# Kernel tuning notes

Measured on AMD Instinct MI355X. Metric: run time of the kernel, lower is better.

## Reference

```python
import jax, jax.numpy as jnp
import numpy as np

DIM = 192
HEADS = 6
WIN = 64  # 8*8
EPS = 1e-12


def setup_inputs() -> dict:
    key = jax.random.key(0)
    ks = jax.random.split(key, 10)
    s = 0.02
    return {
        "qx": jax.random.normal(ks[0], (8192, WIN, DIM), jnp.float32),
        "kvx": jax.random.normal(ks[1], (4096, WIN, DIM), jnp.float32),
        "pos": jax.random.normal(ks[2], (1, WIN, DIM), jnp.float32) * s,
        "Wq": jax.random.normal(ks[3], (DIM, DIM), jnp.float32) * s,
        "bq": jnp.zeros((DIM,), jnp.float32),
        "Wkv": jax.random.normal(ks[4], (2 * DIM, DIM), jnp.float32) * s,
        "bkv": jnp.zeros((2 * DIM,), jnp.float32),
        "Wp": jax.random.normal(ks[5], (DIM, DIM), jnp.float32) * s,
        "bp": jnp.zeros((DIM,), jnp.float32),
    }


def _l2norm(x):
    # F.normalize: x / max(||x||_2, eps) along last dim
    n = jnp.sqrt(jnp.sum(x * x, axis=-1, keepdims=True))
    return x / jnp.maximum(n, EPS)


def reference(qx, kvx, pos, Wq, bq, Wkv, bkv, Wp, bp):
    B_q, q_len, C = qx.shape
    B_kv, kv_len, _ = kvx.shape
    tile_num = B_q // B_kv
    kvx = jnp.tile(kvx, (tile_num, 1, 1))
    qx = qx + pos
    q = qx @ Wq.T + bq                       # [Bq, q, C]
    kv = kvx @ Wkv.T + bkv                   # [Bq, kv, 2C]
    k, v = kv[..., :C], kv[..., C:]
    hd = C // HEADS
    q = q.reshape(B_q, q_len, HEADS, hd).transpose(0, 2, 1, 3)
    k = k.reshape(B_q, kv_len, HEADS, hd).transpose(0, 2, 1, 3)
    v = v.reshape(B_q, kv_len, HEADS, hd).transpose(0, 2, 1, 3)
    scale = 1.0 / np.sqrt(C).astype(np.float32)
    attn = jnp.einsum("bhqd,bhkd->bhqk", _l2norm(q), _l2norm(k)) * scale
    attn = jax.nn.softmax(attn, axis=-1)
    x = jnp.einsum("bhqk,bhkd->bhqd", attn, v)
    x = x.transpose(0, 2, 1, 3).reshape(B_q, q_len, C)
    return x @ Wp.T + bp
```

## Files before the change

### kernel.cpp

```cpp
#include <hip/hip_runtime.h>
#include <hip/hip_bf16.h>

#define TPB   512
#define CDIM  192
#define LDA   200
#define LDST  200
#define SCALE 0.07216878364870323f
#define EPSF  1e-12f

using short8 = __attribute__((ext_vector_type(8))) short;
using f32x4  = __attribute__((ext_vector_type(4))) float;
using us4    = __attribute__((ext_vector_type(4))) unsigned short;

__device__ __forceinline__ unsigned short hc(float f) {
  __hip_bfloat16 h = __float2bfloat16(f);
  unsigned short u; __builtin_memcpy(&u, &h, 2); return u;
}
__device__ __forceinline__ unsigned pack2(float x, float y) {
  return (unsigned)hc(x) | ((unsigned)hc(y) << 16);
}
#define MFMA(a, b, c) __builtin_amdgcn_mfma_f32_16x16x32_bf16((a), (b), (c), 0, 0, 0)
#define SCHED_FENCE() __builtin_amdgcn_sched_barrier(0)

#define NWQ  36864
#define NWKV 73728
#define NWP  36864
__global__ void cvt_weights(const float* __restrict__ Wq, const float* __restrict__ Wkv,
                            const float* __restrict__ Wp, unsigned short* __restrict__ o) {
  int i = blockIdx.x * blockDim.x + threadIdx.x;
  if (i < NWQ) o[i] = hc(Wq[i]);
  else if (i < NWQ + NWKV) o[i] = hc(Wkv[i - NWQ]);
  else if (i < NWQ + NWKV + NWP) o[i] = hc(Wp[i - NWQ - NWKV]);
}

__global__ __launch_bounds__(TPB, 4) void wa_v14(
    const float* __restrict__ qx, const float* __restrict__ kvx,
    const float* __restrict__ pos,
    const float* __restrict__ bq, const float* __restrict__ bkv,
    const float* __restrict__ bp,
    const unsigned short* __restrict__ Wqb, const unsigned short* __restrict__ Wkvb,
    const unsigned short* __restrict__ Wpb,
    float* __restrict__ out, int BKV, int tile_num)
{
  __shared__ __align__(16) unsigned short sA[64 * LDA];
  __shared__ __align__(16) unsigned short sU[64 * LDST];

  const int tid = threadIdx.x;
  const int wid = tid >> 6;
  const int l15 = (tid & 63) & 15;
  const int l4  = (tid & 63) >> 4;
  const int b   = blockIdx.x;
  const size_t kvoff = (size_t)b * (64 * CDIM);

  const int srcA = l15 + 32 * (l4 & 1);
  const int srcB = srcA + 16;
  const int sel  = l4 >> 1;
  auto redistC = [&](f32x4 cA, f32x4 cB) -> short8 {
    unsigned iA0 = pack2(cA[0], cA[1]), iA1 = pack2(cA[2], cA[3]);
    unsigned iB0 = pack2(cB[0], cB[1]), iB1 = pack2(cB[2], cB[3]);
    unsigned A00 = (unsigned)__shfl((int)iA0, srcA);
    unsigned A01 = (unsigned)__shfl((int)iA1, srcA);
    unsigned A10 = (unsigned)__shfl((int)iB0, srcA);
    unsigned A11 = (unsigned)__shfl((int)iB1, srcA);
    unsigned B00 = (unsigned)__shfl((int)iA0, srcB);
    unsigned B01 = (unsigned)__shfl((int)iA1, srcB);
    unsigned B10 = (unsigned)__shfl((int)iB0, srcB);
    unsigned B11 = (unsigned)__shfl((int)iB1, srcB);
    union { uint4 u; short8 s; } uu;
    uu.u.x = sel ? A10 : A00;
    uu.u.y = sel ? A11 : A01;
    uu.u.z = sel ? B10 : B00;
    uu.u.w = sel ? B11 : B01;
    return uu.s;
  };

  auto stage_q = [&](size_t qo) {
    const float4* gq = (const float4*)(qx + qo);
    const float4* p4 = (const float4*)pos;
    #pragma unroll
    for (int t = 0; t < 6; ++t) {
      int e = tid + t * TPB, row = e / 48, c4 = e % 48;
      float4 a = gq[e], p = p4[e];
      us4 wq;
      wq.x = hc(a.x + p.x); wq.y = hc(a.y + p.y); wq.z = hc(a.z + p.z); wq.w = hc(a.w + p.w);
      *(us4*)&sA[row * LDA + c4 * 4] = wq;
    }
  };

  stage_q(kvoff );
  {
    const float4* gk = (const float4*)(kvx + kvoff);
    #pragma unroll
    for (int t = 0; t < 6; ++t) {
      int e = tid + t * TPB, row = e / 48, c4 = e % 48;
      float4 k = gk[e];
      us4 wk; wk.x = hc(k.x); wk.y = hc(k.y); wk.z = hc(k.z); wk.w = hc(k.w);
      *(us4*)&sU[row * LDST + c4 * 4] = wk;
    }
  }
  __syncthreads();

  const int h = wid;

  short8 kres[4];
  short8 av[2][2];
  if (wid < 6) {
    {
      f32x4 kacc[4][2];
      #pragma unroll
      for (int mh = 0; mh < 2; ++mh) {
        float4 bk = *(const float4*)&bkv[32 * h + 16 * mh + 4 * l4];
        #pragma unroll
        for (int n = 0; n < 4; ++n) kacc[n][mh] = f32x4{bk.x, bk.y, bk.z, bk.w};
      }
      #pragma unroll
      for (int ks = 0; ks < 6; ++ks) {
        short8 act[4];
        #pragma unroll
        for (int n = 0; n < 4; ++n)
          act[n] = *(const short8*)&sU[(16 * n + l15) * LDST + ks * 32 + 8 * l4];
        #pragma unroll
        for (int mh = 0; mh < 2; ++mh) {
          short8 kw = *(const short8*)&Wkvb[(size_t)(32 * h + 16 * mh + l15) * CDIM + ks * 32 + 8 * l4];
          #pragma unroll
          for (int n = 0; n < 4; ++n) kacc[n][mh] = MFMA(kw, act[n], kacc[n][mh]);
        }
      }
      #pragma unroll
      for (int n = 0; n < 4; ++n) {
        float ss = 0.f;
        #pragma unroll
        for (int mh = 0; mh < 2; ++mh)
          #pragma unroll
          for (int r = 0; r < 4; ++r) ss += kacc[n][mh][r] * kacc[n][mh][r];
        ss += __shfl_xor(ss, 16);
        ss += __shfl_xor(ss, 32);
        float sc = 1.0f / fmaxf(sqrtf(ss), EPSF);
        #pragma unroll
        for (int mh = 0; mh < 2; ++mh)
          #pragma unroll
          for (int r = 0; r < 4; ++r) kacc[n][mh][r] *= sc;
        kres[n] = redistC(kacc[n][0], kacc[n][1]);
      }
    }
    SCHED_FENCE();
    {
      f32x4 vacc[4][2];
      #pragma unroll
      for (int nv = 0; nv < 2; ++nv) {
        float bv = bkv[CDIM + 32 * h + 16 * nv + l15];
        #pragma unroll
        for (int m = 0; m < 4; ++m) vacc[m][nv] = f32x4{bv, bv, bv, bv};
      }
      #pragma unroll
      for (int ks = 0; ks < 6; ++ks) {
        short8 act[4];
        #pragma unroll
        for (int n = 0; n < 4; ++n)
          act[n] = *(const short8*)&sU[(16 * n + l15) * LDST + ks * 32 + 8 * l4];
        #pragma unroll
        for (int nv = 0; nv < 2; ++nv) {
          short8 vw = *(const short8*)&Wkvb[(size_t)(CDIM + 32 * h + 16 * nv + l15) * CDIM + ks * 32 + 8 * l4];
          #pragma unroll
          for (int m = 0; m < 4; ++m) vacc[m][nv] = MFMA(act[m], vw, vacc[m][nv]);
        }
      }
      #pragma unroll
      for (int cc = 0; cc < 2; ++cc)
        #pragma unroll
        for (int nv = 0; nv < 2; ++nv)
          av[cc][nv] = redistC(vacc[2 * cc][nv], vacc[2 * cc + 1][nv]);
    }
  }
  __syncthreads();

  for (int wq = 0; wq < tile_num; ++wq) {
    const size_t qoff = kvoff + (size_t)wq * BKV * (64 * CDIM);

    if (wid < 6) {
      short8 qres[4];
      {
        f32x4 qacc[4][2];
        #pragma unroll
        for (int mh = 0; mh < 2; ++mh) {
          float4 bk = *(const float4*)&bq[32 * h + 16 * mh + 4 * l4];
          #pragma unroll
          for (int n = 0; n < 4; ++n) qacc[n][mh] = f32x4{bk.x, bk.y, bk.z, bk.w};
        }
        #pragma unroll
        for (int ks = 0; ks < 6; ++ks) {
          short8 act[4];
          #pragma unroll
          for (int n = 0; n < 4; ++n)
            act[n] = *(const short8*)&sA[(16 * n + l15) * LDA + ks * 32 + 8 * l4];
          #pragma unroll
          for (int mh = 0; mh < 2; ++mh) {
            short8 qw = *(const short8*)&Wqb[(size_t)(32 * h + 16 * mh + l15) * CDIM + ks * 32 + 8 * l4];
            #pragma unroll
            for (int n = 0; n < 4; ++n) qacc[n][mh] = MFMA(qw, act[n], qacc[n][mh]);
          }
        }
        #pragma unroll
        for (int n = 0; n < 4; ++n) {
          float ss = 0.f;
          #pragma unroll
          for (int mh = 0; mh < 2; ++mh)
            #pragma unroll
            for (int r = 0; r < 4; ++r) ss += qacc[n][mh][r] * qacc[n][mh][r];
          ss += __shfl_xor(ss, 16);
          ss += __shfl_xor(ss, 32);
          float sc = SCALE / fmaxf(sqrtf(ss), EPSF);
          #pragma unroll
          for (int mh = 0; mh < 2; ++mh)
            #pragma unroll
            for (int r = 0; r < 4; ++r) qacc[n][mh][r] *= sc;
          qres[n] = redistC(qacc[n][0], qacc[n][1]);
        }
      }
      SCHED_FENCE();
      #pragma unroll
      for (int t = 0; t < 4; ++t) {
        f32x4 c[4];
        #pragma unroll
        for (int n = 0; n < 4; ++n) {
          f32x4 z = f32x4{0.f, 0.f, 0.f, 0.f};
          c[n] = MFMA(kres[n], qres[t], z);
        }
        float mx = c[0][0];
        #pragma unroll
        for (int n = 0; n < 4; ++n)
          #pragma unroll
          for (int r = 0; r < 4; ++r) mx = fmaxf(mx, c[n][r]);
        mx = fmaxf(mx, __shfl_xor(mx, 16));
        mx = fmaxf(mx, __shfl_xor(mx, 32));
        float sum = 0.f;
        #pragma unroll
        for (int n = 0; n < 4; ++n)
          #pragma unroll
          for (int r = 0; r < 4; ++r) { c[n][r] = __expf(c[n][r] - mx); sum += c[n][r]; }
        sum += __shfl_xor(sum, 16);
        sum += __shfl_xor(sum, 32);
        const float inv = 1.0f / sum;
        #pragma unroll
        for (int n = 0; n < 4; ++n)
          #pragma unroll
          for (int r = 0; r < 4; ++r) c[n][r] *= inv;
        short8 pa0 = redistC(c[0], c[1]);
        short8 pa1 = redistC(c[2], c[3]);
        f32x4 cx0 = f32x4{0.f, 0.f, 0.f, 0.f};
        f32x4 cx1 = f32x4{0.f, 0.f, 0.f, 0.f};
        cx0 = MFMA(av[0][0], pa0, cx0);
        cx0 = MFMA(av[1][0], pa1, cx0);
        cx1 = MFMA(av[0][1], pa0, cx1);
        cx1 = MFMA(av[1][1], pa1, cx1);
        short8 xf = redistC(cx0, cx1);
        *(short8*)&sU[(16 * t + l15) * LDST + h * 32 + 8 * l4] = xf;
      }
    }
    __syncthreads();

    {
      const int n0 = wid;
      f32x4 oacc[4];
      float bv = bp[n0 * 16 + l15];
      #pragma unroll
      for (int m = 0; m < 4; ++m) oacc[m] = f32x4{bv, bv, bv, bv};
      #pragma unroll
      for (int ks = 0; ks < 6; ++ks) {
        short8 pw = *(const short8*)&Wpb[(size_t)(n0 * 16 + l15) * CDIM + ks * 32 + 8 * l4];
        #pragma unroll
        for (int m = 0; m < 4; ++m) {
          short8 xa = *(const short8*)&sU[(16 * m + l15) * LDST + ks * 32 + 8 * l4];
          oacc[m] = MFMA(xa, pw, oacc[m]);
        }
      }
      #pragma unroll
      for (int m = 0; m < 4; ++m)
        #pragma unroll
        for (int r = 0; r < 4; ++r)
          out[qoff + (size_t)(16 * m + 4 * l4 + r) * CDIM + n0 * 16 + l15] = oacc[m][r];

      SCHED_FENCE();
      if (wid < 4) {
        const int n1 = wid + 8;
        f32x4 oacc2[4];
        float bv2 = bp[n1 * 16 + l15];
        #pragma unroll
        for (int m = 0; m < 4; ++m) oacc2[m] = f32x4{bv2, bv2, bv2, bv2};
        #pragma unroll
        for (int ks = 0; ks < 6; ++ks) {
          short8 pw = *(const short8*)&Wpb[(size_t)(n1 * 16 + l15) * CDIM + ks * 32 + 8 * l4];
          #pragma unroll
          for (int m = 0; m < 4; ++m) {
            short8 xa = *(const short8*)&sU[(16 * m + l15) * LDST + ks * 32 + 8 * l4];
            oacc2[m] = MFMA(xa, pw, oacc2[m]);
          }
        }
        #pragma unroll
        for (int m = 0; m < 4; ++m)
          #pragma unroll
          for (int r = 0; r < 4; ++r)
            out[qoff + (size_t)(16 * m + 4 * l4 + r) * CDIM + n1 * 16 + l15] = oacc2[m][r];
      }
      if (wq + 1 < tile_num)
        stage_q(kvoff + (size_t)(wq + 1) * BKV * (64 * CDIM));
    }
    __syncthreads();
  }
}

extern "C" void kernel_launch(void* const* d_in, const int* in_sizes, int n_in,
                              void* d_out, int out_size, void* d_ws, size_t ws_size,
                              hipStream_t stream) {
  const float* qx  = (const float*)d_in[0];
  const float* kvx = (const float*)d_in[1];
  const float* pos = (const float*)d_in[2];
  const float* Wq  = (const float*)d_in[3];
  const float* bq  = (const float*)d_in[4];
  const float* Wkv = (const float*)d_in[5];
  const float* bkv = (const float*)d_in[6];
  const float* Wp  = (const float*)d_in[7];
  const float* bp  = (const float*)d_in[8];
  float* out = (float*)d_out;
  unsigned short* wsb = (unsigned short*)d_ws;

  const int BQ  = in_sizes[0] / (64 * CDIM);
  const int BKV = in_sizes[1] / (64 * CDIM);
  const int tile_num = BQ / BKV;

  const int ncvt = NWQ + NWKV + NWP;
  cvt_weights<<<(ncvt + 255) / 256, 256, 0, stream>>>(Wq, Wkv, Wp, wsb);

  wa_v14<<<BKV, TPB, 0, stream>>>(qx, kvx, pos, bq, bkv, bp,
                                  wsb, wsb + NWQ, wsb + NWQ + NWKV, out, BKV, tile_num);
}
```

Measured before the change: 574.7 us.

## Register-prefetch next Q tile and recompute K/V per query tile

Loads the next query tile from global memory into registers before the output projection, so the load latency overlaps the projection MFMAs. It then converts and writes the tile to LDS at the start of the next iteration, using separate LDS buffers for the Q/attention data and the KV data. K and V are now recomputed inside the tile loop instead of once per block, which adds MFMA work in exchange for fewer live registers held across iterations. The output-projection split across waves is rebalanced so waves 4-7 take the extra column blocks instead of waves 0-3.

```diff
diff --git a/kernel.cpp b/kernel.cpp
--- a/kernel.cpp
+++ b/kernel.cpp
@@ -3,8 +3,7 @@
 
 #define TPB   512
 #define CDIM  192
-#define LDA   200
-#define LDST  200
+#define LD    200
 #define SCALE 0.07216878364870323f
 #define EPSF  1e-12f
 
@@ -33,7 +32,7 @@
   else if (i < NWQ + NWKV + NWP) o[i] = hc(Wp[i - NWQ - NWKV]);
 }
 
-__global__ __launch_bounds__(TPB, 4) void wa_v14(
+__global__ __launch_bounds__(TPB, 4) void wa_v15(
     const float* __restrict__ qx, const float* __restrict__ kvx,
     const float* __restrict__ pos,
     const float* __restrict__ bq, const float* __restrict__ bkv,
@@ -42,8 +41,8 @@
     const unsigned short* __restrict__ Wpb,
     float* __restrict__ out, int BKV, int tile_num)
 {
-  __shared__ __align__(16) unsigned short sA[64 * LDA];
-  __shared__ __align__(16) unsigned short sU[64 * LDST];
+  __shared__ __align__(16) unsigned short sQX[64 * LD];
+  __shared__ __align__(16) unsigned short sKV[64 * LD];
 
   const int tid = threadIdx.x;
   const int wid = tid >> 6;
@@ -74,56 +73,132 @@
     return uu.s;
   };
 
-  auto stage_q = [&](size_t qo) {
-    const float4* gq = (const float4*)(qx + qo);
-    const float4* p4 = (const float4*)pos;
+  const int h = wid;
+
+  float4 pre[6];
+  {
+    const float4* gq = (const float4*)(qx + kvoff);
     #pragma unroll
-    for (int t = 0; t < 6; ++t) {
-      int e = tid + t * TPB, row = e / 48, c4 = e % 48;
-      float4 a = gq[e], p = p4[e];
-      us4 wq;
-      wq.x = hc(a.x + p.x); wq.y = hc(a.y + p.y); wq.z = hc(a.z + p.z); wq.w = hc(a.w + p.w);
-      *(us4*)&sA[row * LDA + c4 * 4] = wq;
-    }
-  };
-
-  stage_q(kvoff );
-  {
+    for (int t = 0; t < 6; ++t) pre[t] = gq[tid + t * TPB];
     const float4* gk = (const float4*)(kvx + kvoff);
     #pragma unroll
     for (int t = 0; t < 6; ++t) {
       int e = tid + t * TPB, row = e / 48, c4 = e % 48;
       float4 k = gk[e];
       us4 wk; wk.x = hc(k.x); wk.y = hc(k.y); wk.z = hc(k.z); wk.w = hc(k.w);
-      *(us4*)&sU[row * LDST + c4 * 4] = wk;
+      *(us4*)&sKV[row * LD + c4 * 4] = wk;
     }
   }
   __syncthreads();
 
-  const int h = wid;
-
-  short8 kres[4];
-  short8 av[2][2];
-  if (wid < 6) {
+  for (int w = 0; w < tile_num; ++w) {
+    const size_t qoff = kvoff + (size_t)w * BKV * (64 * CDIM);
+
     {
-      f32x4 kacc[4][2];
+      const float4* p4 = (const float4*)pos;
+      #pragma unroll
+      for (int t = 0; t < 6; ++t) {
+        int e = tid + t * TPB, row = e / 48, c4 = e % 48;
+        float4 p = p4[e];
+        us4 wq;
+        wq.x = hc(pre[t].x + p.x); wq.y = hc(pre[t].y + p.y);
+        wq.z = hc(pre[t].z + p.z); wq.w = hc(pre[t].w + p.w);
+        *(us4*)&sQX[row * LD + c4 * 4] = wq;
+      }
+    }
+
+    short8 kres[4];
+    short8 av[2][2];
+    if (wid < 6) {
+      {
+        f32x4 kacc[4][2];
+        #pragma unroll
+        for (int mh = 0; mh < 2; ++mh) {
+          float4 bk = *(const float4*)&bkv[32 * h + 16 * mh + 4 * l4];
+          #pragma unroll
+          for (int n = 0; n < 4; ++n) kacc[n][mh] = f32x4{bk.x, bk.y, bk.z, bk.w};
+        }
+        #pragma unroll
+        for (int ks = 0; ks < 6; ++ks) {
+          short8 act[4];
+          #pragma unroll
+          for (int n = 0; n < 4; ++n)
+            act[n] = *(const short8*)&sKV[(16 * n + l15) * LD + ks * 32 + 8 * l4];
+          #pragma unroll
+          for (int mh = 0; mh < 2; ++mh) {
+            short8 kw = *(const short8*)&Wkvb[(size_t)(32 * h + 16 * mh + l15) * CDIM + ks * 32 + 8 * l4];
+            #pragma unroll
+            for (int n = 0; n < 4; ++n) kacc[n][mh] = MFMA(kw, act[n], kacc[n][mh]);
+          }
+        }
+        #pragma unroll
+        for (int n = 0; n < 4; ++n) {
+          float ss = 0.f;
+          #pragma unroll
+          for (int mh = 0; mh < 2; ++mh)
+            #pragma unroll
+            for (int r = 0; r < 4; ++r) ss += kacc[n][mh][r] * kacc[n][mh][r];
+          ss += __shfl_xor(ss, 16);
+          ss += __shfl_xor(ss, 32);
+          float sc = 1.0f / fmaxf(sqrtf(ss), EPSF);
+          #pragma unroll
+          for (int mh = 0; mh < 2; ++mh)
+            #pragma unroll
+            for (int r = 0; r < 4; ++r) kacc[n][mh][r] *= sc;
+          kres[n] = redistC(kacc[n][0], kacc[n][1]);
+        }
+      }
+      SCHED_FENCE();
+      {
+        f32x4 vacc[4][2];
+        #pragma unroll
+        for (int nv = 0; nv < 2; ++nv) {
+          float bv = bkv[CDIM + 32 * h + 16 * nv + l15];
+          #pragma unroll
+          for (int m = 0; m < 4; ++m) vacc[m][nv] = f32x4{bv, bv, bv, bv};
+        }
+        #pragma unroll
+        for (int ks = 0; ks < 6; ++ks) {
+          short8 act[4];
+          #pragma unroll
+          for (int n = 0; n < 4; ++n)
+            act[n] = *(const short8*)&sKV[(16 * n + l15) * LD + ks * 32 + 8 * l4];
+          #pragma unroll
+          for (int nv = 0; nv < 2; ++nv) {
+            short8 vw = *(const short8*)&Wkvb[(size_t)(CDIM + 32 * h + 16 * nv + l15) * CDIM + ks * 32 + 8 * l4];
+            #pragma unroll
+            for (int m = 0; m < 4; ++m) vacc[m][nv] = MFMA(act[m], vw, vacc[m][nv]);
+          }
+        }
+        #pragma unroll
+        for (int cc = 0; cc < 2; ++cc)
+          #pragma unroll
+          for (int nv = 0; nv < 2; ++nv)
+            av[cc][nv] = redistC(vacc[2 * cc][nv], vacc[2 * cc + 1][nv]);
+      }
+    }
+    __syncthreads();
+
+    short8 qres[4];
+    if (wid < 6) {
+      f32x4 qacc[4][2];
       #pragma unroll
       for (int mh = 0; mh < 2; ++mh) {
-        float4 bk = *(const float4*)&bkv[32 * h + 16 * mh + 4 * l4];
-        #pragma unroll
-        for (int n = 0; n < 4; ++n) kacc[n][mh] = f32x4{bk.x, bk.y, bk.z, bk.w};
+        float4 bk = *(const float4*)&bq[32 * h + 16 * mh + 4 * l4];
+        #pragma unroll
+        for (int n = 0; n < 4; ++n) qacc[n][mh] = f32x4{bk.x, bk.y, bk.z, bk.w};
       }
       #pragma unroll
       for (int ks = 0; ks < 6; ++ks) {
         short8 act[4];
         #pragma unroll
         for (int n = 0; n < 4; ++n)
-          act[n] = *(const short8*)&sU[(16 * n + l15) * LDST + ks * 32 + 8 * l4];
+          act[n] = *(const short8*)&sQX[(16 * n + l15) * LD + ks * 32 + 8 * l4];
         #pragma unroll
         for (int mh = 0; mh < 2; ++mh) {
-          short8 kw = *(const short8*)&Wkvb[(size_t)(32 * h + 16 * mh + l15) * CDIM + ks * 32 + 8 * l4];
-          #pragma unroll
-          for (int n = 0; n < 4; ++n) kacc[n][mh] = MFMA(kw, act[n], kacc[n][mh]);
+          short8 qw = *(const short8*)&Wqb[(size_t)(32 * h + 16 * mh + l15) * CDIM + ks * 32 + 8 * l4];
+          #pragma unroll
+          for (int n = 0; n < 4; ++n) qacc[n][mh] = MFMA(qw, act[n], qacc[n][mh]);
         }
       }
       #pragma unroll
@@ -132,92 +207,20 @@
         #pragma unroll
         for (int mh = 0; mh < 2; ++mh)
           #pragma unroll
-          for (int r = 0; r < 4; ++r) ss += kacc[n][mh][r] * kacc[n][mh][r];
+          for (int r = 0; r < 4; ++r) ss += qacc[n][mh][r] * qacc[n][mh][r];
         ss += __shfl_xor(ss, 16);
         ss += __shfl_xor(ss, 32);
-        float sc = 1.0f / fmaxf(sqrtf(ss), EPSF);
+        float sc = SCALE / fmaxf(sqrtf(ss), EPSF);
         #pragma unroll
         for (int mh = 0; mh < 2; ++mh)
           #pragma unroll
-          for (int r = 0; r < 4; ++r) kacc[n][mh][r] *= sc;
-        kres[n] = redistC(kacc[n][0], kacc[n][1]);
-      }
-    }
-    SCHED_FENCE();
-    {
-      f32x4 vacc[4][2];
-      #pragma unroll
-      for (int nv = 0; nv < 2; ++nv) {
-        float bv = bkv[CDIM + 32 * h + 16 * nv + l15];
-        #pragma unroll
-        for (int m = 0; m < 4; ++m) vacc[m][nv] = f32x4{bv, bv, bv, bv};
-      }
-      #pragma unroll
-      for (int ks = 0; ks < 6; ++ks) {
-        short8 act[4];
-        #pragma unroll
-        for (int n = 0; n < 4; ++n)
-          act[n] = *(const short8*)&sU[(16 * n + l15) * LDST + ks * 32 + 8 * l4];
-        #pragma unroll
-        for (int nv = 0; nv < 2; ++nv) {
-          short8 vw = *(const short8*)&Wkvb[(size_t)(CDIM + 32 * h + 16 * nv + l15) * CDIM + ks * 32 + 8 * l4];
-          #pragma unroll
-          for (int m = 0; m < 4; ++m) vacc[m][nv] = MFMA(act[m], vw, vacc[m][nv]);
-        }
-      }
-      #pragma unroll
-      for (int cc = 0; cc < 2; ++cc)
-        #pragma unroll
-        for (int nv = 0; nv < 2; ++nv)
-          av[cc][nv] = redistC(vacc[2 * cc][nv], vacc[2 * cc + 1][nv]);
-    }
-  }
-  __syncthreads();
-
-  for (int wq = 0; wq < tile_num; ++wq) {
-    const size_t qoff = kvoff + (size_t)wq * BKV * (64 * CDIM);
+          for (int r = 0; r < 4; ++r) qacc[n][mh][r] *= sc;
+        qres[n] = redistC(qacc[n][0], qacc[n][1]);
+      }
+    }
+    __syncthreads();
 
     if (wid < 6) {
-      short8 qres[4];
-      {
-        f32x4 qacc[4][2];
-        #pragma unroll
-        for (int mh = 0; mh < 2; ++mh) {
-          float4 bk = *(const float4*)&bq[32 * h + 16 * mh + 4 * l4];
-          #pragma unroll
-          for (int n = 0; n < 4; ++n) qacc[n][mh] = f32x4{bk.x, bk.y, bk.z, bk.w};
-        }
-        #pragma unroll
-        for (int ks = 0; ks < 6; ++ks) {
-          short8 act[4];
-          #pragma unroll
-          for (int n = 0; n < 4; ++n)
-            act[n] = *(const short8*)&sA[(16 * n + l15) * LDA + ks * 32 + 8 * l4];
-          #pragma unroll
-          for (int mh = 0; mh < 2; ++mh) {
-            short8 qw = *(const short8*)&Wqb[(size_t)(32 * h + 16 * mh + l15) * CDIM + ks * 32 + 8 * l4];
-            #pragma unroll
-            for (int n = 0; n < 4; ++n) qacc[n][mh] = MFMA(qw, act[n], qacc[n][mh]);
-          }
-        }
-        #pragma unroll
-        for (int n = 0; n < 4; ++n) {
-          float ss = 0.f;
-          #pragma unroll
-          for (int mh = 0; mh < 2; ++mh)
-            #pragma unroll
-            for (int r = 0; r < 4; ++r) ss += qacc[n][mh][r] * qacc[n][mh][r];
-          ss += __shfl_xor(ss, 16);
-          ss += __shfl_xor(ss, 32);
-          float sc = SCALE / fmaxf(sqrtf(ss), EPSF);
-          #pragma unroll
-          for (int mh = 0; mh < 2; ++mh)
-            #pragma unroll
-            for (int r = 0; r < 4; ++r) qacc[n][mh][r] *= sc;
-          qres[n] = redistC(qacc[n][0], qacc[n][1]);
-        }
-      }
-      SCHED_FENCE();
       #pragma unroll
       for (int t = 0; t < 4; ++t) {
         f32x4 c[4];
@@ -254,56 +257,60 @@
         cx1 = MFMA(av[0][1], pa0, cx1);
         cx1 = MFMA(av[1][1], pa1, cx1);
         short8 xf = redistC(cx0, cx1);
-        *(short8*)&sU[(16 * t + l15) * LDST + h * 32 + 8 * l4] = xf;
+        *(short8*)&sQX[(16 * t + l15) * LD + h * 32 + 8 * l4] = xf;
       }
     }
     __syncthreads();
 
     {
-      const int n0 = wid;
-      f32x4 oacc[4];
-      float bv = bp[n0 * 16 + l15];
-      #pragma unroll
-      for (int m = 0; m < 4; ++m) oacc[m] = f32x4{bv, bv, bv, bv};
-      #pragma unroll
-      for (int ks = 0; ks < 6; ++ks) {
-        short8 pw = *(const short8*)&Wpb[(size_t)(n0 * 16 + l15) * CDIM + ks * 32 + 8 * l4];
-        #pragma unroll
-        for (int m = 0; m < 4; ++m) {
-          short8 xa = *(const short8*)&sU[(16 * m + l15) * LDST + ks * 32 + 8 * l4];
-          oacc[m] = MFMA(xa, pw, oacc[m]);
-        }
-      }
-      #pragma unroll
-      for (int m = 0; m < 4; ++m)
-        #pragma unroll
-        for (int r = 0; r < 4; ++r)
-          out[qoff + (size_t)(16 * m + 4 * l4 + r) * CDIM + n0 * 16 + l15] = oacc[m][r];
-
+      if (w + 1 < tile_num) {
+        const float4* gq = (const float4*)(qx + qoff + (size_t)BKV * (64 * CDIM));
+        #pragma unroll
+        for (int t = 0; t < 6; ++t) pre[t] = gq[tid + t * TPB];
+      }
+      {
+        const int n0 = wid;
+        f32x4 oacc[4];
+        float bv = bp[n0 * 16 + l15];
+        #pragma unroll
+        for (int m = 0; m < 4; ++m) oacc[m] = f32x4{bv, bv, bv, bv};
+        #pragma unroll
+        for (int ks = 0; ks < 6; ++ks) {
+          short8 pw = *(const short8*)&Wpb[(size_t)(n0 * 16 + l15) * CDIM + ks * 32 + 8 * l4];
+          #pragma unroll
+          for (int m = 0; m < 4; ++m) {
+            short8 xa = *(const short8*)&sQX[(16 * m + l15) * LD + ks * 32 + 8 * l4];
+            oacc[m] = MFMA(xa, pw, oacc[m]);
+          }
+        }
+        #pragma unroll
+        for (int m = 0; m < 4; ++m)
+          #pragma unroll
+          for (int r = 0; r < 4; ++r)
+            out[qoff + (size_t)(16 * m + 4 * l4 + r) * CDIM + n0 * 16 + l15] = oacc[m][r];
+      }
       SCHED_FENCE();
-      if (wid < 4) {
-        const int n1 = wid + 8;
-        f32x4 oacc2[4];
-        float bv2 = bp[n1 * 16 + l15];
-        #pragma unroll
-        for (int m = 0; m < 4; ++m) oacc2[m] = f32x4{bv2, bv2, bv2, bv2};
+      if (wid >= 4) {
+        const int n1 = wid + 4;
+        f32x4 oacc[4];
+        float bv = bp[n1 * 16 + l15];
+        #pragma unroll
+        for (int m = 0; m < 4; ++m) oacc[m] = f32x4{bv, bv, bv, bv};
         #pragma unroll
         for (int ks = 0; ks < 6; ++ks) {
           short8 pw = *(const short8*)&Wpb[(size_t)(n1 * 16 + l15) * CDIM + ks * 32 + 8 * l4];
           #pragma unroll
           for (int m = 0; m < 4; ++m) {
-            short8 xa = *(const short8*)&sU[(16 * m + l15) * LDST + ks * 32 + 8 * l4];
-            oacc2[m] = MFMA(xa, pw, oacc2[m]);
+            short8 xa = *(const short8*)&sQX[(16 * m + l15) * LD + ks * 32 + 8 * l4];
+            oacc[m] = MFMA(xa, pw, oacc[m]);
           }
         }
         #pragma unroll
         for (int m = 0; m < 4; ++m)
           #pragma unroll
           for (int r = 0; r < 4; ++r)
-            out[qoff + (size_t)(16 * m + 4 * l4 + r) * CDIM + n1 * 16 + l15] = oacc2[m][r];
-      }
-      if (wq + 1 < tile_num)
-        stage_q(kvoff + (size_t)(wq + 1) * BKV * (64 * CDIM));
+            out[qoff + (size_t)(16 * m + 4 * l4 + r) * CDIM + n1 * 16 + l15] = oacc[m][r];
+      }
     }
     __syncthreads();
   }
@@ -331,6 +338,6 @@
   const int ncvt = NWQ + NWKV + NWP;
   cvt_weights<<<(ncvt + 255) / 256, 256, 0, stream>>>(Wq, Wkv, Wp, wsb);
 
-  wa_v14<<<BKV, TPB, 0, stream>>>(qx, kvx, pos, bq, bkv, bp,
+  wa_v15<<<BKV, TPB, 0, stream>>>(qx, kvx, pos, bq, bkv, bp,
                                   wsb, wsb + NWQ, wsb + NWQ + NWKV, out, BKV, tile_num);
 }
```

Result: slower. 906.4 us (+57.7%).
